# Kernel optimization log

Hardware: AMD Instinct MI355X
Metric: run time of the kernel (lower is better)

## Reference

```python
import jax, jax.numpy as jnp
import numpy as np

NUM_RANGES = 256
DOPPLER = 64
EMBED = 16
MAX_ELE = 37
MAX_AZI = 107
K_PER_RANGE = 512
IN_DIM = DOPPLER + 2 * EMBED  # 96


def setup_inputs() -> dict:
    key = jax.random.key(0)
    ks = jax.random.split(key, 12)
    N = NUM_RANGES * K_PER_RANGE
    s = 1.0 / np.sqrt(IN_DIM)  # torch Linear default init scale
    return {
        "power_vals": jax.random.normal(ks[0], (N, DOPPLER), dtype=jnp.float32),
        "ele_indices": jax.random.randint(ks[1], (N,), 0, MAX_ELE, dtype=jnp.int32),
        "range_indices": jax.random.randint(ks[2], (N,), 0, NUM_RANGES, dtype=jnp.int32),
        "azi_indices": jax.random.randint(ks[3], (N,), 0, MAX_AZI, dtype=jnp.int32),
        "ele_table": jax.random.normal(ks[4], (MAX_ELE, EMBED), dtype=jnp.float32),
        "azi_table": jax.random.normal(ks[5], (MAX_AZI, EMBED), dtype=jnp.float32),
        "Wq": jax.random.uniform(ks[6], (DOPPLER, IN_DIM), jnp.float32, -s, s),
        "bq": jax.random.uniform(ks[7], (DOPPLER,), jnp.float32, -s, s),
        "Wk": jax.random.uniform(ks[8], (DOPPLER, IN_DIM), jnp.float32, -s, s),
        "bk": jax.random.uniform(ks[9], (DOPPLER,), jnp.float32, -s, s),
        "Wv": jax.random.uniform(ks[10], (DOPPLER, IN_DIM), jnp.float32, -s, s),
        "bv": jax.random.uniform(ks[11], (DOPPLER,), jnp.float32, -s, s),
    }


def reference(power_vals, ele_indices, range_indices, azi_indices,
              ele_table, azi_table, Wq, bq, Wk, bk, Wv, bv):
    Kp = power_vals.shape[0] // NUM_RANGES
    # embedding gather + concat: [R, K, D + 2E]
    ele_e = ele_table[ele_indices.reshape(NUM_RANGES, Kp)]
    azi_e = azi_table[azi_indices.reshape(NUM_RANGES, Kp)]
    pv = power_vals.reshape(NUM_RANGES, Kp, DOPPLER)
    x = jnp.concatenate([pv, ele_e, azi_e], axis=-1)
    # QKV projections (torch Linear: x @ W.T + b)
    Q = jnp.einsum('rkf,df->rkd', x, Wq) + bq
    Kt = jnp.einsum('rkf,df->rkd', x, Wk) + bk
    V = jnp.einsum('rkf,df->rkd', x, Wv) + bv
    scores = jnp.einsum('rqd,rkd->rqk', Q, Kt) / jnp.sqrt(jnp.float32(DOPPLER))
    attn = jax.nn.softmax(scores, axis=-1)
    attended = jnp.einsum('rqk,rkd->rqd', attn, V)
    attended_sum = attended.sum(axis=-1)  # [R, K]
    return attended_sum.reshape(-1)
```

## Files before the change

### kernel.cpp

```cpp
#include <hip/hip_runtime.h>


#define SCALE 0.18033688011112042f

typedef __bf16 bf16;
typedef bf16 v4bf __attribute__((ext_vector_type(4)));
typedef bf16 v8bf __attribute__((ext_vector_type(8)));
typedef float v4f __attribute__((ext_vector_type(4)));

__device__ __forceinline__ v8bf pk8(float4 a, float4 b) {
    v8bf r;
    r[0] = (bf16)a.x; r[1] = (bf16)a.y; r[2] = (bf16)a.z; r[3] = (bf16)a.w;
    r[4] = (bf16)b.x; r[5] = (bf16)b.y; r[6] = (bf16)b.z; r[7] = (bf16)b.w;
    return r;
}
__device__ __forceinline__ float d4(float4 a, v4f w) {
    return a.x * w[0] + a.y * w[1] + a.z * w[2] + a.w * w[3];
}

__global__ __launch_bounds__(1024, 4)
void sda_kernel(const float* __restrict__ power,
                const int*   __restrict__ ele_i,
                const int*   __restrict__ azi_i,
                const float* __restrict__ ele_t,
                const float* __restrict__ azi_t,
                const float* __restrict__ Wq, const float* __restrict__ bq,
                const float* __restrict__ Wk, const float* __restrict__ bk,
                const float* __restrict__ Wv, const float* __restrict__ bv,
                float* __restrict__ out)
{
    extern __shared__ char smem[];
    char*  Kb   = smem;
    float* vsum = (float*)(smem + 65536);
    float* wvs  = (float*)(smem + 67584);
    bf16*  WqL  = (bf16*)(smem + 68096);
    bf16*  WkL  = (bf16*)(smem + 80384);
    float* bqL  = (float*)(smem + 92672);
    float* bkL  = (float*)(smem + 92928);

    const int tid  = threadIdx.x;
    const int wave = tid >> 6;
    const int lane = tid & 63;
    const int l15  = lane & 15;
    const int quad = lane >> 4;
    const int rowbase = blockIdx.x * 512 + wave * 32;

    float4 A[2][4];
    int IE[2], IA[2];
#pragma unroll
    for (int mt = 0; mt < 2; mt++) {
        int row = rowbase + mt * 16 + l15;
        const float* pr = power + (size_t)row * 64;
        A[mt][0] = *(const float4*)(pr + quad * 8);
        A[mt][1] = *(const float4*)(pr + quad * 8 + 4);
        A[mt][2] = *(const float4*)(pr + 32 + quad * 8);
        A[mt][3] = *(const float4*)(pr + 32 + quad * 8 + 4);
        IE[mt] = ele_i[row];
        IA[mt] = azi_i[row];
    }

#pragma unroll
    for (int i = 0; i < 6; i++) {
        int idx = tid + i * 1024;
        WqL[idx] = (bf16)Wq[idx];
        WkL[idx] = (bf16)Wk[idx];
    }
    if (tid < 64) { bqL[tid] = bq[tid]; bkL[tid] = bk[tid]; }
    if (tid < 96) {
        float s = 0.f;
#pragma unroll 16
        for (int r = 0; r < 64; r++) s += Wv[r * 96 + tid];
        wvs[tid] = s;
    } else if (tid == 96) {
        float s = 0.f;
#pragma unroll
        for (int d = 0; d < 64; d++) s += bv[d];
        wvs[96] = s;
    }
    __syncthreads();

    v4f w0 = *(const v4f*)(wvs + quad * 8);
    v4f w1 = *(const v4f*)(wvs + quad * 8 + 4);
    v4f w2 = *(const v4f*)(wvs + 32 + quad * 8);
    v4f w3 = *(const v4f*)(wvs + 32 + quad * 8 + 4);
    v4f w4 = *(const v4f*)(wvs + 64 + quad * 8);
    v4f w5 = *(const v4f*)(wvs + 64 + quad * 8 + 4);
    const float bvs = wvs[96];

    v8bf xa[2][3];
#pragma unroll
    for (int mt = 0; mt < 2; mt++) {
        const float* tb = (quad < 2) ? (ele_t + IE[mt] * 16 + quad * 8)
                                     : (azi_t + IA[mt] * 16 + (quad - 2) * 8);
        float4 a4 = *(const float4*)tb;
        float4 a5 = *(const float4*)(tb + 4);
        xa[mt][0] = pk8(A[mt][0], A[mt][1]);
        xa[mt][1] = pk8(A[mt][2], A[mt][3]);
        xa[mt][2] = pk8(a4, a5);
        float d = d4(A[mt][0], w0) + d4(A[mt][1], w1) + d4(A[mt][2], w2)
                + d4(A[mt][3], w3) + d4(a4, w4) + d4(a5, w5);
        d += __shfl_xor(d, 16);
        d += __shfl_xor(d, 32);
        if (quad == 0) vsum[wave * 32 + mt * 16 + l15] = d + bvs;
    }

    char* Sw = Kb + wave * 4096;
#pragma unroll 1
    for (int mtd = 0; mtd < 4; mtd++) {
        const bf16* wrow = WqL + (mtd * 16 + l15) * 96;
        v8bf wq3[3];
#pragma unroll
        for (int kt = 0; kt < 3; kt++)
            wq3[kt] = *(const v8bf*)(wrow + kt * 32 + quad * 8);
        float4 bq4 = *(const float4*)(bqL + mtd * 16 + quad * 4);
#pragma unroll
        for (int ntr = 0; ntr < 2; ntr++) {
            v4f acc = {0.f, 0.f, 0.f, 0.f};
#pragma unroll
            for (int kt = 0; kt < 3; kt++)
                acc = __builtin_amdgcn_mfma_f32_16x16x32_bf16(wq3[kt], xa[ntr][kt], acc, 0, 0, 0);
            int row = ntr * 16 + l15;
            v4bf o;
            o[0] = (bf16)((acc[0] + bq4.x) * SCALE);
            o[1] = (bf16)((acc[1] + bq4.y) * SCALE);
            o[2] = (bf16)((acc[2] + bq4.z) * SCALE);
            o[3] = (bf16)((acc[3] + bq4.w) * SCALE);
            *(v4bf*)(Sw + row * 128 +
                     ((((mtd * 2 + (quad >> 1)) ^ (row & 7)) << 4) | ((quad & 1) << 3))) = o;
        }
    }
    v8bf qf[2][2];
#pragma unroll
    for (int nt = 0; nt < 2; nt++)
#pragma unroll
        for (int kt = 0; kt < 2; kt++)
            qf[nt][kt] = *(const v8bf*)(Sw + (nt * 16 + l15) * 128 +
                                        (((kt * 4 + quad) ^ (l15 & 7)) << 4));

#pragma unroll 1
    for (int mtd = 0; mtd < 4; mtd++) {
        const bf16* wrow = WkL + (mtd * 16 + l15) * 96;
        v8bf wk3[3];
#pragma unroll
        for (int kt = 0; kt < 3; kt++)
            wk3[kt] = *(const v8bf*)(wrow + kt * 32 + quad * 8);
        float4 bk4 = *(const float4*)(bkL + mtd * 16 + quad * 4);
#pragma unroll
        for (int ntr = 0; ntr < 2; ntr++) {
            v4f acc = {0.f, 0.f, 0.f, 0.f};
#pragma unroll
            for (int kt = 0; kt < 3; kt++)
                acc = __builtin_amdgcn_mfma_f32_16x16x32_bf16(wk3[kt], xa[ntr][kt], acc, 0, 0, 0);
            int keyb = wave * 32 + ntr * 16 + l15;
            v4bf o;
            o[0] = (bf16)(acc[0] + bk4.x);
            o[1] = (bf16)(acc[1] + bk4.y);
            o[2] = (bf16)(acc[2] + bk4.z);
            o[3] = (bf16)(acc[3] + bk4.w);
            *(v4bf*)(Kb + keyb * 128 +
                     ((((mtd * 2 + (quad >> 1)) ^ (keyb & 7)) << 4) | ((quad & 1) << 3))) = o;
        }
    }
    __syncthreads();

    float osum[2] = {0.f, 0.f};
    float lsum[2] = {0.f, 0.f};
#pragma unroll 2
    for (int t = 0; t < 16; t++) {
        v8bf kf[2][2];
#pragma unroll
        for (int mtk = 0; mtk < 2; mtk++)
#pragma unroll
            for (int kt = 0; kt < 2; kt++) {
                int key = t * 32 + mtk * 16 + l15;
                kf[mtk][kt] = *(const v8bf*)(Kb + key * 128 + (((kt * 4 + quad) ^ (key & 7)) << 4));
            }
        v4f vs[2];
#pragma unroll
        for (int mtk = 0; mtk < 2; mtk++)
            vs[mtk] = *(const v4f*)(vsum + t * 32 + mtk * 16 + quad * 4);
#pragma unroll
        for (int mtk = 0; mtk < 2; mtk++) {
#pragma unroll
            for (int nt = 0; nt < 2; nt++) {
                v4f acc = {0.f, 0.f, 0.f, 0.f};
                acc = __builtin_amdgcn_mfma_f32_16x16x32_bf16(kf[mtk][0], qf[nt][0], acc, 0, 0, 0);
                acc = __builtin_amdgcn_mfma_f32_16x16x32_bf16(kf[mtk][1], qf[nt][1], acc, 0, 0, 0);
                float p0 = __builtin_amdgcn_exp2f(acc[0]);
                float p1 = __builtin_amdgcn_exp2f(acc[1]);
                float p2 = __builtin_amdgcn_exp2f(acc[2]);
                float p3 = __builtin_amdgcn_exp2f(acc[3]);
                lsum[nt] += (p0 + p1) + (p2 + p3);
                osum[nt] += ((p0 * vs[mtk][0] + p1 * vs[mtk][1]) +
                             (p2 * vs[mtk][2] + p3 * vs[mtk][3]));
            }
        }
    }

#pragma unroll
    for (int nt = 0; nt < 2; nt++) {
        float lv = lsum[nt];
        lv += __shfl_xor(lv, 16);
        lv += __shfl_xor(lv, 32);
        float ov = osum[nt];
        ov += __shfl_xor(ov, 16);
        ov += __shfl_xor(ov, 32);
        if (quad == 0) out[rowbase + nt * 16 + l15] = ov / lv;
    }
}

extern "C" void kernel_launch(void* const* d_in, const int* in_sizes, int n_in,
                              void* d_out, int out_size, void* d_ws, size_t ws_size,
                              hipStream_t stream) {
    const float* power = (const float*)d_in[0];
    const int*   ele_i = (const int*)d_in[1];
    const int*   azi_i = (const int*)d_in[3];
    const float* ele_t = (const float*)d_in[4];
    const float* azi_t = (const float*)d_in[5];
    const float* Wq = (const float*)d_in[6];
    const float* bq = (const float*)d_in[7];
    const float* Wk = (const float*)d_in[8];
    const float* bk = (const float*)d_in[9];
    const float* Wv = (const float*)d_in[10];
    const float* bv = (const float*)d_in[11];
    float* out = (float*)d_out;

    const int lds_bytes = 93184;
    (void)hipFuncSetAttribute(reinterpret_cast<const void*>(sda_kernel),
                              hipFuncAttributeMaxDynamicSharedMemorySize, lds_bytes);
    sda_kernel<<<256, 1024, lds_bytes, stream>>>(power, ele_i, azi_i, ele_t, azi_t,
                                                 Wq, bq, Wk, bk, Wv, bv, out);
}
```

Baseline: 110.7 us.

## Double-buffer key tiles in attention loop and parallelize Wv column sums

The attention loop now software-pipelines loads of key fragments and V-sums into two register buffers, so LDS reads for the next tile overlap the MFMA and exp work on the current one. It also uses packed two-wide float accumulators to encourage packed FMA instructions. The Wv column-sum reduction is split across 768 threads in two stages through LDS instead of 96 threads each summing 64 rows serially. Embedding-table gathers are issued earlier to hide latency. The changes add register pressure and an extra barrier.

```diff
diff --git a/kernel.cpp b/kernel.cpp
--- a/kernel.cpp
+++ b/kernel.cpp
@@ -7,6 +7,7 @@
 typedef bf16 v4bf __attribute__((ext_vector_type(4)));
 typedef bf16 v8bf __attribute__((ext_vector_type(8)));
 typedef float v4f __attribute__((ext_vector_type(4)));
+typedef float v2f __attribute__((ext_vector_type(2)));
 
 __device__ __forceinline__ v8bf pk8(float4 a, float4 b) {
     v8bf r;
@@ -37,6 +38,7 @@
     bf16*  WkL  = (bf16*)(smem + 80384);
     float* bqL  = (float*)(smem + 92672);
     float* bkL  = (float*)(smem + 92928);
+    float* pbuf = (float*)smem;
 
     const int tid  = threadIdx.x;
     const int wave = tid >> 6;
@@ -45,18 +47,29 @@
     const int quad = lane >> 4;
     const int rowbase = blockIdx.x * 512 + wave * 32;
 
+    int IE[2], IA[2];
+#pragma unroll
+    for (int mt = 0; mt < 2; mt++) {
+        int row = rowbase + mt * 16 + l15;
+        IE[mt] = ele_i[row];
+        IA[mt] = azi_i[row];
+    }
     float4 A[2][4];
-    int IE[2], IA[2];
-#pragma unroll
-    for (int mt = 0; mt < 2; mt++) {
-        int row = rowbase + mt * 16 + l15;
-        const float* pr = power + (size_t)row * 64;
+#pragma unroll
+    for (int mt = 0; mt < 2; mt++) {
+        const float* pr = power + (size_t)(rowbase + mt * 16 + l15) * 64;
         A[mt][0] = *(const float4*)(pr + quad * 8);
         A[mt][1] = *(const float4*)(pr + quad * 8 + 4);
         A[mt][2] = *(const float4*)(pr + 32 + quad * 8);
         A[mt][3] = *(const float4*)(pr + 32 + quad * 8 + 4);
-        IE[mt] = ele_i[row];
-        IA[mt] = azi_i[row];
+    }
+    float4 T0[2], T1[2];
+#pragma unroll
+    for (int mt = 0; mt < 2; mt++) {
+        const float* tb = (quad < 2) ? (ele_t + IE[mt] * 16 + quad * 8)
+                                     : (azi_t + IA[mt] * 16 + (quad - 2) * 8);
+        T0[mt] = *(const float4*)tb;
+        T1[mt] = *(const float4*)(tb + 4);
     }
 
 #pragma unroll
@@ -65,16 +78,27 @@
         WqL[idx] = (bf16)Wq[idx];
         WkL[idx] = (bf16)Wk[idx];
     }
+    if (tid < 768) {
+        int c = tid % 96;
+        int g = tid / 96;
+        float s = 0.f;
+#pragma unroll
+        for (int r = 0; r < 8; r++) s += Wv[(g * 8 + r) * 96 + c];
+        pbuf[g * 96 + c] = s;
+    } else if (tid < 832) {
+        pbuf[768 + (tid - 768)] = bv[tid - 768];
+    }
     if (tid < 64) { bqL[tid] = bq[tid]; bkL[tid] = bk[tid]; }
+    __syncthreads();
     if (tid < 96) {
         float s = 0.f;
-#pragma unroll 16
-        for (int r = 0; r < 64; r++) s += Wv[r * 96 + tid];
+#pragma unroll
+        for (int g = 0; g < 8; g++) s += pbuf[g * 96 + tid];
         wvs[tid] = s;
     } else if (tid == 96) {
         float s = 0.f;
 #pragma unroll
-        for (int d = 0; d < 64; d++) s += bv[d];
+        for (int j = 0; j < 64; j++) s += pbuf[768 + j];
         wvs[96] = s;
     }
     __syncthreads();
@@ -90,15 +114,11 @@
     v8bf xa[2][3];
 #pragma unroll
     for (int mt = 0; mt < 2; mt++) {
-        const float* tb = (quad < 2) ? (ele_t + IE[mt] * 16 + quad * 8)
-                                     : (azi_t + IA[mt] * 16 + (quad - 2) * 8);
-        float4 a4 = *(const float4*)tb;
-        float4 a5 = *(const float4*)(tb + 4);
         xa[mt][0] = pk8(A[mt][0], A[mt][1]);
         xa[mt][1] = pk8(A[mt][2], A[mt][3]);
-        xa[mt][2] = pk8(a4, a5);
+        xa[mt][2] = pk8(T0[mt], T1[mt]);
         float d = d4(A[mt][0], w0) + d4(A[mt][1], w1) + d4(A[mt][2], w2)
-                + d4(A[mt][3], w3) + d4(a4, w4) + d4(a5, w5);
+                + d4(A[mt][3], w3) + d4(T0[mt], w4) + d4(T1[mt], w5);
         d += __shfl_xor(d, 16);
         d += __shfl_xor(d, 32);
         if (quad == 0) vsum[wave * 32 + mt * 16 + l15] = d + bvs;
@@ -163,50 +183,69 @@
     }
     __syncthreads();
 
-    float osum[2] = {0.f, 0.f};
-    float lsum[2] = {0.f, 0.f};
-#pragma unroll 2
-    for (int t = 0; t < 16; t++) {
-        v8bf kf[2][2];
-#pragma unroll
-        for (int mtk = 0; mtk < 2; mtk++)
-#pragma unroll
-            for (int kt = 0; kt < 2; kt++) {
-                int key = t * 32 + mtk * 16 + l15;
-                kf[mtk][kt] = *(const v8bf*)(Kb + key * 128 + (((kt * 4 + quad) ^ (key & 7)) << 4));
-            }
-        v4f vs[2];
-#pragma unroll
-        for (int mtk = 0; mtk < 2; mtk++)
-            vs[mtk] = *(const v4f*)(vsum + t * 32 + mtk * 16 + quad * 4);
-#pragma unroll
-        for (int mtk = 0; mtk < 2; mtk++) {
-#pragma unroll
-            for (int nt = 0; nt < 2; nt++) {
-                v4f acc = {0.f, 0.f, 0.f, 0.f};
-                acc = __builtin_amdgcn_mfma_f32_16x16x32_bf16(kf[mtk][0], qf[nt][0], acc, 0, 0, 0);
-                acc = __builtin_amdgcn_mfma_f32_16x16x32_bf16(kf[mtk][1], qf[nt][1], acc, 0, 0, 0);
-                float p0 = __builtin_amdgcn_exp2f(acc[0]);
-                float p1 = __builtin_amdgcn_exp2f(acc[1]);
-                float p2 = __builtin_amdgcn_exp2f(acc[2]);
-                float p3 = __builtin_amdgcn_exp2f(acc[3]);
-                lsum[nt] += (p0 + p1) + (p2 + p3);
-                osum[nt] += ((p0 * vs[mtk][0] + p1 * vs[mtk][1]) +
-                             (p2 * vs[mtk][2] + p3 * vs[mtk][3]));
-            }
-        }
-    }
+#define LOADT(t, K, V)                                                          \
+    {                                                                           \
+        _Pragma("unroll")                                                       \
+        for (int mtk = 0; mtk < 2; mtk++) {                                     \
+            int key = (t) * 32 + mtk * 16 + l15;                                \
+            _Pragma("unroll")                                                   \
+            for (int kt = 0; kt < 2; kt++)                                      \
+                K[mtk][kt] = *(const v8bf*)(Kb + key * 128 +                    \
+                             (((kt * 4 + quad) ^ (key & 7)) << 4));             \
+            V[mtk] = *(const v4f*)(vsum + (t) * 32 + mtk * 16 + quad * 4);      \
+        }                                                                       \
+    }
+
+#define COMPUTE(K, V)                                                           \
+    {                                                                           \
+        _Pragma("unroll")                                                       \
+        for (int mtk = 0; mtk < 2; mtk++) {                                     \
+            v2f v01 = {V[mtk][0], V[mtk][1]};                                   \
+            v2f v23 = {V[mtk][2], V[mtk][3]};                                   \
+            _Pragma("unroll")                                                   \
+            for (int nt = 0; nt < 2; nt++) {                                    \
+                v4f acc = {0.f, 0.f, 0.f, 0.f};                                 \
+                acc = __builtin_amdgcn_mfma_f32_16x16x32_bf16(K[mtk][0], qf[nt][0], acc, 0, 0, 0); \
+                acc = __builtin_amdgcn_mfma_f32_16x16x32_bf16(K[mtk][1], qf[nt][1], acc, 0, 0, 0); \
+                v2f p01 = {__builtin_amdgcn_exp2f(acc[0]),                      \
+                           __builtin_amdgcn_exp2f(acc[1])};                     \
+                v2f p23 = {__builtin_amdgcn_exp2f(acc[2]),                      \
+                           __builtin_amdgcn_exp2f(acc[3])};                     \
+                lacc[nt] += p01 + p23;                        \
+                oacc[nt] += p01 * v01 + p23 * v23;            \
+            }                                                                   \
+        }                                                                       \
+    }
+
+    v8bf kA[2][2], kB[2][2];
+    v4f  vA[2], vB[2];
+    v2f lacc[2] = {{0.f, 0.f}, {0.f, 0.f}};
+    v2f oacc[2] = {{0.f, 0.f}, {0.f, 0.f}};
+
+    LOADT(0, kA, vA);
+#pragma unroll 1
+    for (int tp = 0; tp < 7; tp++) {
+        LOADT(2 * tp + 1, kB, vB);
+        COMPUTE(kA, vA);
+        LOADT(2 * tp + 2, kA, vA);
+        COMPUTE(kB, vB);
+    }
+    LOADT(15, kB, vB);
+    COMPUTE(kA, vA);
+    COMPUTE(kB, vB);
 
 #pragma unroll
     for (int nt = 0; nt < 2; nt++) {
-        float lv = lsum[nt];
+        float lv = lacc[nt][0] + lacc[nt][1];
         lv += __shfl_xor(lv, 16);
         lv += __shfl_xor(lv, 32);
-        float ov = osum[nt];
+        float ov = oacc[nt][0] + oacc[nt][1];
         ov += __shfl_xor(ov, 16);
         ov += __shfl_xor(ov, 32);
         if (quad == 0) out[rowbase + nt * 16 + l15] = ov / lv;
     }
+#undef LOADT
+#undef COMPUTE
 }
 
 extern "C" void kernel_launch(void* const* d_in, const int* in_sizes, int n_in,
```

New measurement: 110.7 us. No clear change (+0.0%).

## Halve attention waves so each reuses K fragments for 64 queries

Applied to the files above, without the earlier changes.

In the attention phase only 8 of 16 waves remain active, and each handles 64 query rows instead of 32. Every K fragment read from LDS is then reused across four query tiles, halving total LDS K traffic. The change also parallelises the Wv column-sum reduction across 768 threads, issues the embedding-table loads early so they overlap the weight staging, and accumulates with packed float2 math. In exchange it adds two extra block barriers and idles half the waves during the exp/MFMA loop, which may reduce latency hiding.

```diff
diff --git a/kernel.cpp b/kernel.cpp
--- a/kernel.cpp
+++ b/kernel.cpp
@@ -7,6 +7,7 @@
 typedef bf16 v4bf __attribute__((ext_vector_type(4)));
 typedef bf16 v8bf __attribute__((ext_vector_type(8)));
 typedef float v4f __attribute__((ext_vector_type(4)));
+typedef float v2f __attribute__((ext_vector_type(2)));
 
 __device__ __forceinline__ v8bf pk8(float4 a, float4 b) {
     v8bf r;
@@ -37,6 +38,7 @@
     bf16*  WkL  = (bf16*)(smem + 80384);
     float* bqL  = (float*)(smem + 92672);
     float* bkL  = (float*)(smem + 92928);
+    float* pbuf = (float*)smem;
 
     const int tid  = threadIdx.x;
     const int wave = tid >> 6;
@@ -45,18 +47,29 @@
     const int quad = lane >> 4;
     const int rowbase = blockIdx.x * 512 + wave * 32;
 
+    int IE[2], IA[2];
+#pragma unroll
+    for (int mt = 0; mt < 2; mt++) {
+        int row = rowbase + mt * 16 + l15;
+        IE[mt] = ele_i[row];
+        IA[mt] = azi_i[row];
+    }
     float4 A[2][4];
-    int IE[2], IA[2];
-#pragma unroll
-    for (int mt = 0; mt < 2; mt++) {
-        int row = rowbase + mt * 16 + l15;
-        const float* pr = power + (size_t)row * 64;
+#pragma unroll
+    for (int mt = 0; mt < 2; mt++) {
+        const float* pr = power + (size_t)(rowbase + mt * 16 + l15) * 64;
         A[mt][0] = *(const float4*)(pr + quad * 8);
         A[mt][1] = *(const float4*)(pr + quad * 8 + 4);
         A[mt][2] = *(const float4*)(pr + 32 + quad * 8);
         A[mt][3] = *(const float4*)(pr + 32 + quad * 8 + 4);
-        IE[mt] = ele_i[row];
-        IA[mt] = azi_i[row];
+    }
+    float4 T0[2], T1[2];
+#pragma unroll
+    for (int mt = 0; mt < 2; mt++) {
+        const float* tb = (quad < 2) ? (ele_t + IE[mt] * 16 + quad * 8)
+                                     : (azi_t + IA[mt] * 16 + (quad - 2) * 8);
+        T0[mt] = *(const float4*)tb;
+        T1[mt] = *(const float4*)(tb + 4);
     }
 
 #pragma unroll
@@ -65,16 +78,27 @@
         WqL[idx] = (bf16)Wq[idx];
         WkL[idx] = (bf16)Wk[idx];
     }
+    if (tid < 768) {
+        int c = tid % 96;
+        int g = tid / 96;
+        float s = 0.f;
+#pragma unroll
+        for (int r = 0; r < 8; r++) s += Wv[(g * 8 + r) * 96 + c];
+        pbuf[g * 96 + c] = s;
+    } else if (tid < 832) {
+        pbuf[768 + (tid - 768)] = bv[tid - 768];
+    }
     if (tid < 64) { bqL[tid] = bq[tid]; bkL[tid] = bk[tid]; }
+    __syncthreads();
     if (tid < 96) {
         float s = 0.f;
-#pragma unroll 16
-        for (int r = 0; r < 64; r++) s += Wv[r * 96 + tid];
+#pragma unroll
+        for (int g = 0; g < 8; g++) s += pbuf[g * 96 + tid];
         wvs[tid] = s;
     } else if (tid == 96) {
         float s = 0.f;
 #pragma unroll
-        for (int d = 0; d < 64; d++) s += bv[d];
+        for (int j = 0; j < 64; j++) s += pbuf[768 + j];
         wvs[96] = s;
     }
     __syncthreads();
@@ -90,15 +114,11 @@
     v8bf xa[2][3];
 #pragma unroll
     for (int mt = 0; mt < 2; mt++) {
-        const float* tb = (quad < 2) ? (ele_t + IE[mt] * 16 + quad * 8)
-                                     : (azi_t + IA[mt] * 16 + (quad - 2) * 8);
-        float4 a4 = *(const float4*)tb;
-        float4 a5 = *(const float4*)(tb + 4);
         xa[mt][0] = pk8(A[mt][0], A[mt][1]);
         xa[mt][1] = pk8(A[mt][2], A[mt][3]);
-        xa[mt][2] = pk8(a4, a5);
+        xa[mt][2] = pk8(T0[mt], T1[mt]);
         float d = d4(A[mt][0], w0) + d4(A[mt][1], w1) + d4(A[mt][2], w2)
-                + d4(A[mt][3], w3) + d4(a4, w4) + d4(a5, w5);
+                + d4(A[mt][3], w3) + d4(T0[mt], w4) + d4(T1[mt], w5);
         d += __shfl_xor(d, 16);
         d += __shfl_xor(d, 32);
         if (quad == 0) vsum[wave * 32 + mt * 16 + l15] = d + bvs;
@@ -129,13 +149,22 @@
                      ((((mtd * 2 + (quad >> 1)) ^ (row & 7)) << 4) | ((quad & 1) << 3))) = o;
         }
     }
-    v8bf qf[2][2];
-#pragma unroll
-    for (int nt = 0; nt < 2; nt++)
-#pragma unroll
-        for (int kt = 0; kt < 2; kt++)
-            qf[nt][kt] = *(const v8bf*)(Sw + (nt * 16 + l15) * 128 +
-                                        (((kt * 4 + quad) ^ (l15 & 7)) << 4));
+    __syncthreads();
+
+    v8bf qf[4][2];
+    if (wave < 8) {
+#pragma unroll
+        for (int g = 0; g < 2; g++) {
+            const char* base = Kb + (wave + 8 * g) * 4096;
+#pragma unroll
+            for (int nt = 0; nt < 2; nt++)
+#pragma unroll
+                for (int kt = 0; kt < 2; kt++)
+                    qf[g * 2 + nt][kt] = *(const v8bf*)(base + (nt * 16 + l15) * 128 +
+                                                        (((kt * 4 + quad) ^ (l15 & 7)) << 4));
+        }
+    }
+    __syncthreads();
 
 #pragma unroll 1
     for (int mtd = 0; mtd < 4; mtd++) {
@@ -163,9 +192,11 @@
     }
     __syncthreads();
 
-    float osum[2] = {0.f, 0.f};
-    float lsum[2] = {0.f, 0.f};
-#pragma unroll 2
+    if (wave >= 8) return;
+
+    v2f lacc[4] = {{0.f,0.f},{0.f,0.f},{0.f,0.f},{0.f,0.f}};
+    v2f oacc[4] = {{0.f,0.f},{0.f,0.f},{0.f,0.f},{0.f,0.f}};
+#pragma unroll 1
     for (int t = 0; t < 16; t++) {
         v8bf kf[2][2];
 #pragma unroll
@@ -181,31 +212,33 @@
             vs[mtk] = *(const v4f*)(vsum + t * 32 + mtk * 16 + quad * 4);
 #pragma unroll
         for (int mtk = 0; mtk < 2; mtk++) {
-#pragma unroll
-            for (int nt = 0; nt < 2; nt++) {
+            v2f v01 = {vs[mtk][0], vs[mtk][1]};
+            v2f v23 = {vs[mtk][2], vs[mtk][3]};
+#pragma unroll
+            for (int qg = 0; qg < 4; qg++) {
                 v4f acc = {0.f, 0.f, 0.f, 0.f};
-                acc = __builtin_amdgcn_mfma_f32_16x16x32_bf16(kf[mtk][0], qf[nt][0], acc, 0, 0, 0);
-                acc = __builtin_amdgcn_mfma_f32_16x16x32_bf16(kf[mtk][1], qf[nt][1], acc, 0, 0, 0);
-                float p0 = __builtin_amdgcn_exp2f(acc[0]);
-                float p1 = __builtin_amdgcn_exp2f(acc[1]);
-                float p2 = __builtin_amdgcn_exp2f(acc[2]);
-                float p3 = __builtin_amdgcn_exp2f(acc[3]);
-                lsum[nt] += (p0 + p1) + (p2 + p3);
-                osum[nt] += ((p0 * vs[mtk][0] + p1 * vs[mtk][1]) +
-                             (p2 * vs[mtk][2] + p3 * vs[mtk][3]));
+                acc = __builtin_amdgcn_mfma_f32_16x16x32_bf16(kf[mtk][0], qf[qg][0], acc, 0, 0, 0);
+                acc = __builtin_amdgcn_mfma_f32_16x16x32_bf16(kf[mtk][1], qf[qg][1], acc, 0, 0, 0);
+                v2f p01 = {__builtin_amdgcn_exp2f(acc[0]), __builtin_amdgcn_exp2f(acc[1])};
+                v2f p23 = {__builtin_amdgcn_exp2f(acc[2]), __builtin_amdgcn_exp2f(acc[3])};
+                lacc[qg] += p01 + p23;
+                oacc[qg] += p01 * v01 + p23 * v23;
             }
         }
     }
 
 #pragma unroll
-    for (int nt = 0; nt < 2; nt++) {
-        float lv = lsum[nt];
+    for (int qg = 0; qg < 4; qg++) {
+        float lv = lacc[qg][0] + lacc[qg][1];
         lv += __shfl_xor(lv, 16);
         lv += __shfl_xor(lv, 32);
-        float ov = osum[nt];
+        float ov = oacc[qg][0] + oacc[qg][1];
         ov += __shfl_xor(ov, 16);
         ov += __shfl_xor(ov, 32);
-        if (quad == 0) out[rowbase + nt * 16 + l15] = ov / lv;
+        if (quad == 0) {
+            int row = blockIdx.x * 512 + (wave + 8 * (qg >> 1)) * 32 + (qg & 1) * 16 + l15;
+            out[row] = ov / lv;
+        }
     }
 }
 
```

Result: no change. 112.5 us (+1.6%).
